# Kernel tuning notes

Measured on AMD Instinct MI355X. Metric: run time of the kernel, lower is better.

The kernel has to match this reference:

```python
import jax, jax.numpy as jnp
import numpy as np

B, T, D_MODEL, H = 2, 2048, 1024, 16
D_HEAD = D_MODEL // H


def setup_inputs() -> dict:
    key = jax.random.key(0)
    k1, k2, k3 = jax.random.split(key, 3)
    x = jax.random.normal(k1, (B, T, D_MODEL), dtype=jnp.float32)
    # Linear weights stored as (in, out); scale like torch default init roughly
    W_qkv = jax.random.normal(k2, (D_MODEL, 3 * D_MODEL), dtype=jnp.float32) / np.sqrt(D_MODEL)
    W_o = jax.random.normal(k3, (D_MODEL, D_MODEL), dtype=jnp.float32) / np.sqrt(D_MODEL)
    return {"x": x, "W_qkv": W_qkv, "W_o": W_o}


def reference(x, W_qkv, W_o):
    Bx, Tx, C = x.shape
    qkv = x @ W_qkv                                   # (B,T,3C)
    qkv = qkv.reshape(Bx, Tx, 3, H, D_HEAD)
    q = qkv[:, :, 0].transpose(0, 2, 1, 3)            # (B,H,T,D)
    k = qkv[:, :, 1].transpose(0, 2, 1, 3)
    v = qkv[:, :, 2].transpose(0, 2, 1, 3)
    scale = 1.0 / np.sqrt(D_HEAD).astype(np.float32)
    att = jnp.einsum('bhqd,bhkd->bhqk', q, k) * scale  # (B,H,T,T)
    causal = jnp.tril(jnp.ones((Tx, Tx), dtype=bool))
    att = jnp.where(causal[None, None], att, jnp.float32(-jnp.inf))
    w = jax.nn.softmax(att, axis=-1)
    out = jnp.einsum('bhqk,bhkd->bhqd', w, v)          # (B,H,T,D)
    out = out.transpose(0, 2, 1, 3).reshape(Bx, Tx, C)
    return out @ W_o
```

## Files before the change

kernel.cpp:

```cpp
#include <hip/hip_runtime.h>

typedef unsigned short u16;
typedef unsigned int u32;
typedef __bf16 bf16x8 __attribute__((ext_vector_type(8)));
typedef float f32x4 __attribute__((ext_vector_type(4)));

#define DEV __device__ __forceinline__

constexpr int BB = 2;
constexpr int TT = 2048;
constexpr int CD = 1024;
constexpr int HH = 16;
constexpr int DH = 64;
constexpr int BT = BB * TT;

#define QSCALE 0.18033688011112042f

DEV u16 f2bf(float f) {
    return __builtin_bit_cast(u16, (__bf16)f);
}

DEV f32x4 mfma16(bf16x8 a, bf16x8 b, f32x4 c) {
    return __builtin_amdgcn_mfma_f32_16x16x32_bf16(a, b, c, 0, 0, 0);
}

DEV void gld_lds16(u16* lds, const u16* g) {
    __builtin_amdgcn_global_load_lds(
        (const __attribute__((address_space(1))) unsigned int*)g,
        (__attribute__((address_space(3))) unsigned int*)lds, 16, 0, 0);
}

__global__ __launch_bounds__(256)
void prep_kernel(const float* __restrict__ x, u16* __restrict__ xb,
                 const float* __restrict__ Wqkv, u16* __restrict__ WqkvT,
                 const float* __restrict__ Wo, u16* __restrict__ WoT) {
    const int tid = threadIdx.x;
    int blk = blockIdx.x;
    if (blk < 2048) {
        const int i = (blk * 256 + tid) * 8;
        float4 a = *(const float4*)&x[i];
        float4 b = *(const float4*)&x[i + 4];
        u16 t[8];
        t[0] = f2bf(a.x); t[1] = f2bf(a.y); t[2] = f2bf(a.z); t[3] = f2bf(a.w);
        t[4] = f2bf(b.x); t[5] = f2bf(b.y); t[6] = f2bf(b.z); t[7] = f2bf(b.w);
        *(uint4*)&xb[i] = *(const uint4*)t;
        return;
    }
    __shared__ u16 tile[32][33];
    const float* in; u16* out; int rows, cols, bx, by;
    if (blk < 5120) { blk -= 2048; in = Wqkv; out = WqkvT; rows = 1024; cols = 3072; bx = blk % 96; by = blk / 96; }
    else            { blk -= 5120; in = Wo;   out = WoT;   rows = 1024; cols = 1024; bx = blk % 32; by = blk / 32; }
    const int c0 = bx * 32, r0 = by * 32;
    const int tx = tid & 31, ty = tid >> 5;
    #pragma unroll
    for (int i = ty; i < 32; i += 8)
        tile[i][tx] = f2bf(in[(r0 + i) * cols + (c0 + tx)]);
    __syncthreads();
    #pragma unroll
    for (int i = ty; i < 32; i += 8)
        out[(c0 + i) * rows + (r0 + tx)] = tile[tx][i];
}

template <int EPI, int BN, int GX>
__global__ __launch_bounds__(256)
void gemm_db(const u16* __restrict__ A, const u16* __restrict__ Bt,
             u16* __restrict__ out0, u16* __restrict__ out1,
             u16* __restrict__ out2, float* __restrict__ outf,
             int M, int N, int K) {
    constexpr int BM = 128, BK = 32, AST = 32;
    constexpr int NT = BN / 32;
    constexpr int NBLK = GX * 32;
    constexpr int CPX = NBLK / 8;
    __shared__ alignas(16) u16 As[3][BM * AST];
    __shared__ alignas(16) u16 Bs[3][BN * AST];

    const int tid  = threadIdx.x;
    const int wave = tid >> 6, lane = tid & 63;
    const int quad = lane >> 4, l16 = lane & 15;
    const int wm = (wave & 1) * 64, wn = (wave >> 1) * (BN / 2);

    int bid = (int)blockIdx.x;
    bid = (bid & 7) * CPX + (bid >> 3);
    const int bx = bid % GX, by = bid / GX;
    const int m0 = by * BM, n0 = bx * BN;

    const int srowA = wave * 32 + (lane >> 2);
    const int srowB = wave * (BN / 4) + (lane >> 2);
    const int scol  = (((lane & 3) ^ ((lane >> 3) & 3))) * 8;
    const u16* ga0 = A  + (size_t)(m0 + srowA) * K + scol;
    const u16* ga1 = ga0 + (size_t)16 * K;
    const u16* gb0 = Bt + (size_t)(n0 + srowB) * K + scol;
    const u16* gb1 = gb0 + (size_t)16 * K;

    auto stage = [&](int buf, int k0) {
        gld_lds16(&As[buf][wave * 1024],           ga0 + k0);
        gld_lds16(&As[buf][wave * 1024 + 512],     ga1 + k0);
        gld_lds16(&Bs[buf][wave * (BN * 8)],       gb0 + k0);
        if constexpr (BN == 128)
            gld_lds16(&Bs[buf][wave * (BN * 8) + 512], gb1 + k0);
    };
    auto wait_lps = [&]() {
        if constexpr (BN == 128) asm volatile("s_waitcnt vmcnt(4)" ::: "memory");
        else                     asm volatile("s_waitcnt vmcnt(3)" ::: "memory");
    };

    f32x4 acc[4][NT] = {};

    stage(0, 0);
    stage(1, BK);
    wait_lps();
    __builtin_amdgcn_s_barrier();

    const int sx = ((l16 >> 1) & 3) * 8;
    const int NS = K / BK;
    int cb = 0;
    for (int t = 0; t < NS; ++t) {
        const bool pf = (t + 2 < NS);
        int sb = cb + 2; if (sb >= 3) sb -= 3;
        if (pf) stage(sb, (t + 2) * BK);

        bf16x8 fa[4], fb[NT];
        #pragma unroll
        for (int mt = 0; mt < 4; ++mt)
            fa[mt] = *(const bf16x8*)
                &As[cb][(wm + mt * 16 + l16) * AST + (quad * 8 ^ sx)];
        #pragma unroll
        for (int nt = 0; nt < NT; ++nt)
            fb[nt] = *(const bf16x8*)
                &Bs[cb][(wn + nt * 16 + l16) * AST + (quad * 8 ^ sx)];
        #pragma unroll
        for (int mt = 0; mt < 4; ++mt)
            #pragma unroll
            for (int nt = 0; nt < NT; ++nt)
                acc[mt][nt] = mfma16(fa[mt], fb[nt], acc[mt][nt]);

        if (pf) wait_lps();
        else    asm volatile("s_waitcnt vmcnt(0)" ::: "memory");
        __builtin_amdgcn_s_barrier();
        cb = (cb + 1 == 3) ? 0 : cb + 1;
    }

    #pragma unroll
    for (int mt = 0; mt < 4; ++mt) {
        #pragma unroll
        for (int nt = 0; nt < NT; ++nt) {
            #pragma unroll
            for (int reg = 0; reg < 4; ++reg) {
                const int r = m0 + wm + mt * 16 + quad * 4 + reg;
                const int c = n0 + wn + nt * 16 + l16;
                if (EPI == 0) {
                    outf[(size_t)r * N + c] = acc[mt][nt][reg];
                } else {
                    const int which = c >> 10;
                    const int cc = c & 1023;
                    const int h = cc >> 6, d = cc & 63;
                    const int b = r >> 11, t = r & 2047;
                    const int bh = b * HH + h;
                    if (which == 0) {
                        out0[((size_t)bh * TT + t) * DH + d] =
                            f2bf(acc[mt][nt][reg] * QSCALE);
                    } else if (which == 1) {
                        out1[((size_t)bh * TT + t) * DH + d] = f2bf(acc[mt][nt][reg]);
                    } else {
                        out2[((size_t)bh * DH + d) * TT + t] = f2bf(acc[mt][nt][reg]);
                    }
                }
            }
        }
    }
}

constexpr int KST = 72;

DEV void attn_step(const bf16x8 fk[4][2], const bf16x8 fv[2][4],
                   const bf16x8* fq, f32x4* Oacc,
                   float& m_i, float& l_i, bool diag,
                   int wave, int quad, int l16) {
    f32x4 st[4];
    #pragma unroll
    for (int nt = 0; nt < 4; ++nt) {
        f32x4 t = {};
        t = mfma16(fk[nt][0], fq[0], t);
        t = mfma16(fk[nt][1], fq[1], t);
        st[nt] = t;
    }

    if (diag) {
        const int qg = wave * 16 + l16;
        #pragma unroll
        for (int nt = 0; nt < 4; ++nt)
            #pragma unroll
            for (int reg = 0; reg < 4; ++reg) {
                const int kg = nt * 16 + quad * 4 + reg;
                st[nt][reg] = (kg <= qg) ? st[nt][reg] : -INFINITY;
            }
    }

    float v[16];
    #pragma unroll
    for (int nt = 0; nt < 4; ++nt)
        #pragma unroll
        for (int reg = 0; reg < 4; ++reg)
            v[nt * 4 + reg] = st[nt][reg];
    #pragma unroll
    for (int s = 8; s > 0; s >>= 1)
        #pragma unroll
        for (int i = 0; i < s; ++i)
            v[i] = fmaxf(v[i], v[i + s]);
    float vmax = v[0];
    vmax = fmaxf(vmax, __shfl_xor(vmax, 16, 64));
    vmax = fmaxf(vmax, __shfl_xor(vmax, 32, 64));

    const float mnew = fmaxf(m_i, vmax);
    const float alpha = __builtin_amdgcn_exp2f(m_i - mnew);
    m_i = mnew;

    #pragma unroll
    for (int nt = 0; nt < 4; ++nt)
        #pragma unroll
        for (int reg = 0; reg < 4; ++reg) {
            const float p = __builtin_amdgcn_exp2f(st[nt][reg] - mnew);
            st[nt][reg] = p;
            v[nt * 4 + reg] = p;
        }
    #pragma unroll
    for (int s = 8; s > 0; s >>= 1)
        #pragma unroll
        for (int i = 0; i < s; ++i)
            v[i] += v[i + s];
    float vsum = v[0];
    vsum += __shfl_xor(vsum, 16, 64);
    vsum += __shfl_xor(vsum, 32, 64);
    l_i = l_i * alpha + vsum;

    #pragma unroll
    for (int dt = 0; dt < 4; ++dt)
        #pragma unroll
        for (int reg = 0; reg < 4; ++reg)
            Oacc[dt][reg] *= alpha;

    #pragma unroll
    for (int pair = 0; pair < 2; ++pair) {
        bf16x8 pb;
        #pragma unroll
        for (int j = 0; j < 4; ++j) {
            pb[j]     = (__bf16)st[2 * pair][j];
            pb[4 + j] = (__bf16)st[2 * pair + 1][j];
        }
        #pragma unroll
        for (int dt = 0; dt < 4; ++dt)
            Oacc[dt] = mfma16(fv[pair][dt], pb, Oacc[dt]);
    }
}

__global__ __launch_bounds__(256, 4)
void attn_kernel(const u16* __restrict__ Q, const u16* __restrict__ Kb,
                 const u16* __restrict__ Vt, u16* __restrict__ O) {
    __shared__ alignas(16) u16 Ks[2][64 * KST];
    __shared__ alignas(16) u16 Vs[2][64 * KST];

    const int bid = (int)blockIdx.x;
    const int j2 = bid >> 3;
    const int qt = 31 - (j2 >> 2);
    const int bh = (bid & 7) + 8 * (j2 & 3);
    const int jmax = qt;

    const int tid = threadIdx.x;
    const int wave = tid >> 6, lane = tid & 63;
    const int quad = lane >> 4, l16 = lane & 15;

    const u16* Qh = Q  + (size_t)bh * TT * DH;
    const u16* Kh = Kb + (size_t)bh * TT * DH;
    const u16* Vh = Vt + (size_t)bh * DH * TT;

    const int row = qt * 64 + wave * 16;

    bf16x8 fq[2];
    fq[0] = *(const bf16x8*)&Qh[(row + l16) * DH + quad * 8];
    fq[1] = *(const bf16x8*)&Qh[(row + l16) * DH + 32 + quad * 8];

    f32x4 Oa[4] = {};
    float m_i = -INFINITY, l_i = 0.f;

    const int trow = tid >> 3;
    const int ic   = tid & 7;
    const int tcol = ic * 8;
    const int vc1 = 32 * (ic >> 2) + 16 * (ic & 1) + 4 * ((ic & 3) >> 1);
    uint4 kr0, kr1, vr0, vr1;

    auto load_chunk = [&](int j) {
        const u16* ks = Kh + (size_t)j * 64 * DH;
        kr0 = *(const uint4*)&ks[trow * DH + tcol];
        kr1 = *(const uint4*)&ks[(trow + 32) * DH + tcol];
        const u16* vs = Vh + (size_t)j * 64;
        vr0 = *(const uint4*)&vs[(size_t)trow * TT + tcol];
        vr1 = *(const uint4*)&vs[(size_t)(trow + 32) * TT + tcol];
    };
    auto write_chunk = [&](int buf) {
        *(uint4*)&Ks[buf][trow * KST + tcol]        = kr0;
        *(uint4*)&Ks[buf][(trow + 32) * KST + tcol] = kr1;
        *(uint2*)&Vs[buf][trow * KST + vc1]            = *(const uint2*)&vr0;
        *(uint2*)&Vs[buf][trow * KST + vc1 + 8]        = *((const uint2*)&vr0 + 1);
        *(uint2*)&Vs[buf][(trow + 32) * KST + vc1]     = *(const uint2*)&vr1;
        *(uint2*)&Vs[buf][(trow + 32) * KST + vc1 + 8] = *((const uint2*)&vr1 + 1);
    };

    load_chunk(0);
    write_chunk(0);

    for (int j = 0; j <= jmax; ++j) {
        const int cur = j & 1;
        __syncthreads();
        if (j < jmax) load_chunk(j + 1);

        bf16x8 fk[4][2], fv[2][4];
        #pragma unroll
        for (int nt = 0; nt < 4; ++nt) {
            fk[nt][0] = *(const bf16x8*)&Ks[cur][(nt * 16 + l16) * KST + quad * 8];
            fk[nt][1] = *(const bf16x8*)&Ks[cur][(nt * 16 + l16) * KST + 32 + quad * 8];
        }
        #pragma unroll
        for (int pair = 0; pair < 2; ++pair)
            #pragma unroll
            for (int dt = 0; dt < 4; ++dt)
                fv[pair][dt] = *(const bf16x8*)
                    &Vs[cur][(dt * 16 + l16) * KST + pair * 32 + quad * 8];

        attn_step(fk, fv, fq, Oa, m_i, l_i, (j == qt), wave, quad, l16);
        if (j < jmax) write_chunk(cur ^ 1);
    }

    const int b = bh >> 4, h = bh & 15;
    const float r_i = 1.f / l_i;
    #pragma unroll
    for (int dt = 0; dt < 4; ++dt) {
        u16 oa[4];
        #pragma unroll
        for (int reg = 0; reg < 4; ++reg)
            oa[reg] = f2bf(Oa[dt][reg] * r_i);
        *(uint2*)&O[((size_t)(b * TT + row + l16)) * CD + h * DH + dt * 16 + quad * 4] =
            *(const uint2*)oa;
    }
}

extern "C" void kernel_launch(void* const* d_in, const int* in_sizes, int n_in,
                              void* d_out, int out_size, void* d_ws, size_t ws_size,
                              hipStream_t stream) {
    (void)in_sizes; (void)n_in; (void)out_size; (void)ws_size;
    const float* x    = (const float*)d_in[0];
    const float* Wqkv = (const float*)d_in[1];
    const float* Wo   = (const float*)d_in[2];
    float* out = (float*)d_out;

    char* ws = (char*)d_ws;
    u16* xb    = (u16*)(ws + 0);
    u16* WqkvT = (u16*)(ws + (8u  << 20));
    u16* WoT   = (u16*)(ws + (14u << 20));
    u16* Qb    = (u16*)(ws + (16u << 20));
    u16* Kb    = (u16*)(ws + (24u << 20));
    u16* Vt    = (u16*)(ws + (32u << 20));
    u16* attn  = (u16*)(ws + (40u << 20));

    prep_kernel<<<6144, 256, 0, stream>>>(x, xb, Wqkv, WqkvT, Wo, WoT);

    gemm_db<1, 128, 24><<<768, 256, 0, stream>>>(
        xb, WqkvT, Qb, Kb, Vt, nullptr, BT, 3072, CD);

    attn_kernel<<<1024, 256, 0, stream>>>(Qb, Kb, Vt, attn);

    gemm_db<0, 64, 16><<<512, 256, 0, stream>>>(
        attn, WoT, nullptr, nullptr, nullptr, out, BT, CD, CD);
}
```

Before: 179.5 us.

## Process two query tiles per attention block to share K/V shared-memory loads

Each attention block now handles two adjacent 64-row query tiles (128 rows) against the same staged K/V chunks. Each K and V fragment read from shared memory therefore feeds MFMAs for both tiles, which halves K/V global and LDS traffic per query row. The grid shrinks from 1024 to 512 blocks, with a new scheduling order that pairs heavy and light causal tiles. Launch bounds drop to 2 waves per SIMD to make room for the doubled register state, which lowers occupancy and latency hiding.

```diff
diff --git a/kernel.cpp b/kernel.cpp
--- a/kernel.cpp
+++ b/kernel.cpp
@@ -172,21 +172,9 @@
 
 constexpr int KST = 72;
 
-DEV void attn_step(const bf16x8 fk[4][2], const bf16x8 fv[2][4],
-                   const bf16x8* fq, f32x4* Oacc,
-                   float& m_i, float& l_i, bool diag,
-                   int wave, int quad, int l16) {
-    f32x4 st[4];
-    #pragma unroll
-    for (int nt = 0; nt < 4; ++nt) {
-        f32x4 t = {};
-        t = mfma16(fk[nt][0], fq[0], t);
-        t = mfma16(fk[nt][1], fq[1], t);
-        st[nt] = t;
-    }
-
+DEV void softmax_half(f32x4* st, f32x4* Oacc, float& m_i, float& l_i,
+                      bool diag, int quad, int qg) {
     if (diag) {
-        const int qg = wave * 16 + l16;
         #pragma unroll
         for (int nt = 0; nt < 4; ++nt)
             #pragma unroll
@@ -195,7 +183,6 @@
                 st[nt][reg] = (kg <= qg) ? st[nt][reg] : -INFINITY;
             }
     }
-
     float v[16];
     #pragma unroll
     for (int nt = 0; nt < 4; ++nt)
@@ -238,32 +225,19 @@
         #pragma unroll
         for (int reg = 0; reg < 4; ++reg)
             Oacc[dt][reg] *= alpha;
-
-    #pragma unroll
-    for (int pair = 0; pair < 2; ++pair) {
-        bf16x8 pb;
-        #pragma unroll
-        for (int j = 0; j < 4; ++j) {
-            pb[j]     = (__bf16)st[2 * pair][j];
-            pb[4 + j] = (__bf16)st[2 * pair + 1][j];
-        }
-        #pragma unroll
-        for (int dt = 0; dt < 4; ++dt)
-            Oacc[dt] = mfma16(fv[pair][dt], pb, Oacc[dt]);
-    }
-}
-
-__global__ __launch_bounds__(256, 4)
+}
+
+__global__ __launch_bounds__(256, 2)
 void attn_kernel(const u16* __restrict__ Q, const u16* __restrict__ Kb,
                  const u16* __restrict__ Vt, u16* __restrict__ O) {
     __shared__ alignas(16) u16 Ks[2][64 * KST];
     __shared__ alignas(16) u16 Vs[2][64 * KST];
 
     const int bid = (int)blockIdx.x;
-    const int j2 = bid >> 3;
-    const int qt = 31 - (j2 >> 2);
-    const int bh = (bid & 7) + 8 * (j2 & 3);
-    const int jmax = qt;
+    const int bh = bid & 31;
+    const int q  = (bid < 256) ? 15 - (bid >> 5) : (bid >> 5) - 8;
+    const int jA = 2 * q;
+    const int jB = 2 * q + 1;
 
     const int tid = threadIdx.x;
     const int wave = tid >> 6, lane = tid & 63;
@@ -273,14 +247,17 @@
     const u16* Kh = Kb + (size_t)bh * TT * DH;
     const u16* Vh = Vt + (size_t)bh * DH * TT;
 
-    const int row = qt * 64 + wave * 16;
-
-    bf16x8 fq[2];
-    fq[0] = *(const bf16x8*)&Qh[(row + l16) * DH + quad * 8];
-    fq[1] = *(const bf16x8*)&Qh[(row + l16) * DH + 32 + quad * 8];
-
-    f32x4 Oa[4] = {};
-    float m_i = -INFINITY, l_i = 0.f;
+    const int rowA = q * 128 + wave * 16;
+    const int rowB = q * 128 + 64 + wave * 16;
+
+    bf16x8 fqA[2], fqB[2];
+    fqA[0] = *(const bf16x8*)&Qh[(rowA + l16) * DH + quad * 8];
+    fqA[1] = *(const bf16x8*)&Qh[(rowA + l16) * DH + 32 + quad * 8];
+    fqB[0] = *(const bf16x8*)&Qh[(rowB + l16) * DH + quad * 8];
+    fqB[1] = *(const bf16x8*)&Qh[(rowB + l16) * DH + 32 + quad * 8];
+
+    f32x4 OaA[4] = {}, OaB[4] = {};
+    float mA = -INFINITY, lA = 0.f, mB = -INFINITY, lB = 0.f;
 
     const int trow = tid >> 3;
     const int ic   = tid & 7;
@@ -308,38 +285,71 @@
     load_chunk(0);
     write_chunk(0);
 
-    for (int j = 0; j <= jmax; ++j) {
+    for (int j = 0; j <= jB; ++j) {
         const int cur = j & 1;
         __syncthreads();
-        if (j < jmax) load_chunk(j + 1);
-
-        bf16x8 fk[4][2], fv[2][4];
+        if (j < jB) load_chunk(j + 1);
+
+        const bool doA = (j <= jA);
+        const u16* Kc = Ks[cur];
+        const u16* Vc = Vs[cur];
+
+        f32x4 sA[4], sB[4];
         #pragma unroll
         for (int nt = 0; nt < 4; ++nt) {
-            fk[nt][0] = *(const bf16x8*)&Ks[cur][(nt * 16 + l16) * KST + quad * 8];
-            fk[nt][1] = *(const bf16x8*)&Ks[cur][(nt * 16 + l16) * KST + 32 + quad * 8];
-        }
-        #pragma unroll
-        for (int pair = 0; pair < 2; ++pair)
-            #pragma unroll
-            for (int dt = 0; dt < 4; ++dt)
-                fv[pair][dt] = *(const bf16x8*)
-                    &Vs[cur][(dt * 16 + l16) * KST + pair * 32 + quad * 8];
-
-        attn_step(fk, fv, fq, Oa, m_i, l_i, (j == qt), wave, quad, l16);
-        if (j < jmax) write_chunk(cur ^ 1);
+            const bf16x8 k0 = *(const bf16x8*)&Kc[(nt * 16 + l16) * KST + quad * 8];
+            const bf16x8 k1 = *(const bf16x8*)&Kc[(nt * 16 + l16) * KST + 32 + quad * 8];
+            if (doA) {
+                f32x4 t = {};
+                t = mfma16(k0, fqA[0], t);
+                t = mfma16(k1, fqA[1], t);
+                sA[nt] = t;
+            }
+            f32x4 u = {};
+            u = mfma16(k0, fqB[0], u);
+            u = mfma16(k1, fqB[1], u);
+            sB[nt] = u;
+        }
+
+        if (doA) softmax_half(sA, OaA, mA, lA, (j == jA), quad, wave * 16 + l16);
+        softmax_half(sB, OaB, mB, lB, (j == jB), quad, wave * 16 + l16);
+
+        #pragma unroll
+        for (int pair = 0; pair < 2; ++pair) {
+            bf16x8 pbA, pbB;
+            #pragma unroll
+            for (int jj = 0; jj < 4; ++jj) {
+                pbA[jj]     = (__bf16)sA[2 * pair][jj];
+                pbA[4 + jj] = (__bf16)sA[2 * pair + 1][jj];
+                pbB[jj]     = (__bf16)sB[2 * pair][jj];
+                pbB[4 + jj] = (__bf16)sB[2 * pair + 1][jj];
+            }
+            #pragma unroll
+            for (int dt = 0; dt < 4; ++dt) {
+                const bf16x8 fvd = *(const bf16x8*)
+                    &Vc[(dt * 16 + l16) * KST + pair * 32 + quad * 8];
+                if (doA) OaA[dt] = mfma16(fvd, pbA, OaA[dt]);
+                OaB[dt] = mfma16(fvd, pbB, OaB[dt]);
+            }
+        }
+
+        if (j < jB) write_chunk(cur ^ 1);
     }
 
     const int b = bh >> 4, h = bh & 15;
-    const float r_i = 1.f / l_i;
+    const float rA = 1.f / lA, rB = 1.f / lB;
     #pragma unroll
     for (int dt = 0; dt < 4; ++dt) {
-        u16 oa[4];
-        #pragma unroll
-        for (int reg = 0; reg < 4; ++reg)
-            oa[reg] = f2bf(Oa[dt][reg] * r_i);
-        *(uint2*)&O[((size_t)(b * TT + row + l16)) * CD + h * DH + dt * 16 + quad * 4] =
+        u16 oa[4], ob[4];
+        #pragma unroll
+        for (int reg = 0; reg < 4; ++reg) {
+            oa[reg] = f2bf(OaA[dt][reg] * rA);
+            ob[reg] = f2bf(OaB[dt][reg] * rB);
+        }
+        *(uint2*)&O[((size_t)(b * TT + rowA + l16)) * CD + h * DH + dt * 16 + quad * 4] =
             *(const uint2*)oa;
+        *(uint2*)&O[((size_t)(b * TT + rowB + l16)) * CD + h * DH + dt * 16 + quad * 4] =
+            *(const uint2*)ob;
     }
 }
 
@@ -366,7 +376,7 @@
     gemm_db<1, 128, 24><<<768, 256, 0, stream>>>(
         xb, WqkvT, Qb, Kb, Vt, nullptr, BT, 3072, CD);
 
-    attn_kernel<<<1024, 256, 0, stream>>>(Qb, Kb, Vt, attn);
+    attn_kernel<<<512, 256, 0, stream>>>(Qb, Kb, Vt, attn);
 
     gemm_db<0, 64, 16><<<512, 256, 0, stream>>>(
         attn, WoT, nullptr, nullptr, nullptr, out, BT, CD, CD);
```

Measured after the change: 181.0 us. About the same (+0.8%).

## Split long causal query tiles across two blocks and merge with a combine kernel

Applied to the files above, without the earlier changes.

Query tiles 16-31 have their key range split in two halves handled by separate blocks that write fp32 partial outputs and running max/sum to workspace. A new combine kernel rescales and merges each pair into the bf16 attention output. A task table orders the work so long and short tiles are paired to balance load across the 1536 blocks. This trades an extra launch and fp32 partial-output traffic for less tail imbalance from the longest causal rows. The split path is used only when the workspace is large enough, otherwise the original kernel runs.

```diff
diff --git a/kernel.cpp b/kernel.cpp
--- a/kernel.cpp
+++ b/kernel.cpp
@@ -172,6 +172,15 @@
 
 constexpr int KST = 72;
 
+__device__ const unsigned char TQT[48] = {
+    31,31,30,15,  30,29,29,28,14,  28,27,27,26,13,  26,25,25,24,12,
+    24,23,23,22,11,  22,21,21,20,10,  20,19,19,18,9,  18,17,17,16,8,
+    16,7,  6,5,4,3,2,1,0};
+__device__ const unsigned char TMODE[48] = {
+    0,1,0,2,  1,0,1,0,2,  1,0,1,0,2,  1,0,1,0,2,
+    1,0,1,0,2,  1,0,1,0,2,  1,0,1,0,2,  1,0,1,0,2,
+    1,2,  2,2,2,2,2,2,2};
+
 DEV void attn_step(const bf16x8 fk[4][2], const bf16x8 fv[2][4],
                    const bf16x8* fq, f32x4* Oacc,
                    float& m_i, float& l_i, bool diag,
@@ -253,17 +262,29 @@
     }
 }
 
+template <int SPLIT>
 __global__ __launch_bounds__(256, 4)
 void attn_kernel(const u16* __restrict__ Q, const u16* __restrict__ Kb,
-                 const u16* __restrict__ Vt, u16* __restrict__ O) {
+                 const u16* __restrict__ Vt, u16* __restrict__ O,
+                 float* __restrict__ Opart, float* __restrict__ MLpart) {
     __shared__ alignas(16) u16 Ks[2][64 * KST];
     __shared__ alignas(16) u16 Vs[2][64 * KST];
 
     const int bid = (int)blockIdx.x;
-    const int j2 = bid >> 3;
-    const int qt = 31 - (j2 >> 2);
-    const int bh = (bid & 7) + 8 * (j2 & 3);
-    const int jmax = qt;
+    int qt, mode, bh;
+    if (SPLIT) {
+        const int task = bid >> 5;
+        qt = TQT[task]; mode = TMODE[task];
+        bh = bid & 31;
+    } else {
+        qt = 31 - (bid >> 5); mode = 2;
+        bh = (bid & 7) + 8 * ((bid >> 3) & 3);
+    }
+    const int c0 = (qt + 2) >> 1;
+    int j0 = 0, j1 = qt;
+    bool hasdiag = true;
+    if (SPLIT && mode == 0) { j1 = c0 - 1; hasdiag = false; }
+    if (SPLIT && mode == 1) { j0 = c0; }
 
     const int tid = threadIdx.x;
     const int wave = tid >> 6, lane = tid & 63;
@@ -305,13 +326,13 @@
         *(uint2*)&Vs[buf][(trow + 32) * KST + vc1 + 8] = *((const uint2*)&vr1 + 1);
     };
 
-    load_chunk(0);
+    load_chunk(j0);
     write_chunk(0);
 
-    for (int j = 0; j <= jmax; ++j) {
-        const int cur = j & 1;
+    for (int j = j0; j <= j1; ++j) {
+        const int cur = (j - j0) & 1;
         __syncthreads();
-        if (j < jmax) load_chunk(j + 1);
+        if (j < j1) load_chunk(j + 1);
 
         bf16x8 fk[4][2], fv[2][4];
         #pragma unroll
@@ -326,27 +347,77 @@
                 fv[pair][dt] = *(const bf16x8*)
                     &Vs[cur][(dt * 16 + l16) * KST + pair * 32 + quad * 8];
 
-        attn_step(fk, fv, fq, Oa, m_i, l_i, (j == qt), wave, quad, l16);
-        if (j < jmax) write_chunk(cur ^ 1);
-    }
-
+        attn_step(fk, fv, fq, Oa, m_i, l_i, hasdiag && (j == qt),
+                  wave, quad, l16);
+        if (j < j1) write_chunk(cur ^ 1);
+    }
+
+    if (!SPLIT || mode == 2) {
+        const int b = bh >> 4, h = bh & 15;
+        const float r_i = 1.f / l_i;
+        #pragma unroll
+        for (int dt = 0; dt < 4; ++dt) {
+            u16 oa[4];
+            #pragma unroll
+            for (int reg = 0; reg < 4; ++reg)
+                oa[reg] = f2bf(Oa[dt][reg] * r_i);
+            *(uint2*)&O[((size_t)(b * TT + row + l16)) * CD + h * DH + dt * 16 + quad * 4] =
+                *(const uint2*)oa;
+        }
+    } else {
+        const int pidx = ((qt - 16) * 32 + bh) * 2 + mode;
+        float* Op = Opart + (size_t)pidx * 4096;
+        #pragma unroll
+        for (int dt = 0; dt < 4; ++dt)
+            #pragma unroll
+            for (int reg = 0; reg < 4; ++reg)
+                Op[(dt * 16 + quad * 4 + reg) * 64 + wave * 16 + l16] = Oa[dt][reg];
+        if (quad == 0) {
+            MLpart[pidx * 128 + wave * 16 + l16]      = m_i;
+            MLpart[pidx * 128 + 64 + wave * 16 + l16] = l_i;
+        }
+    }
+}
+
+__global__ __launch_bounds__(256)
+void attn_combine(const float* __restrict__ Opart,
+                  const float* __restrict__ MLpart, u16* __restrict__ O) {
+    const int pair = (int)blockIdx.x;
+    const int qti = pair >> 5, bh = pair & 31;
+    const int qt = 16 + qti;
+    const int pbase = (qti * 32 + bh) * 2;
+    const float* O0 = Opart + (size_t)pbase * 4096;
+    const float* O1 = O0 + 4096;
+    const float* ml0 = MLpart + pbase * 128;
+    const float* ml1 = ml0 + 128;
+
+    const int tid = threadIdx.x;
+    const int rrow = tid >> 2;
+    const int d0 = (tid & 3) * 16;
+
+    const float m0 = ml0[rrow], l0 = ml0[64 + rrow];
+    const float m1 = ml1[rrow], l1 = ml1[64 + rrow];
+    const float M = fmaxf(m0, m1);
+    const float w0 = __builtin_amdgcn_exp2f(m0 - M);
+    const float w1 = __builtin_amdgcn_exp2f(m1 - M);
+    const float rL = 1.f / (l0 * w0 + l1 * w1);
+
+    u16 o[16];
+    #pragma unroll
+    for (int i = 0; i < 16; ++i) {
+        const int d = d0 + i;
+        o[i] = f2bf((O0[d * 64 + rrow] * w0 + O1[d * 64 + rrow] * w1) * rL);
+    }
     const int b = bh >> 4, h = bh & 15;
-    const float r_i = 1.f / l_i;
-    #pragma unroll
-    for (int dt = 0; dt < 4; ++dt) {
-        u16 oa[4];
-        #pragma unroll
-        for (int reg = 0; reg < 4; ++reg)
-            oa[reg] = f2bf(Oa[dt][reg] * r_i);
-        *(uint2*)&O[((size_t)(b * TT + row + l16)) * CD + h * DH + dt * 16 + quad * 4] =
-            *(const uint2*)oa;
-    }
+    u16* dst = &O[((size_t)(b * TT + qt * 64 + rrow)) * CD + h * DH + d0];
+    *(uint4*)dst = *(const uint4*)o;
+    *(uint4*)(dst + 8) = *((const uint4*)o + 1);
 }
 
 extern "C" void kernel_launch(void* const* d_in, const int* in_sizes, int n_in,
                               void* d_out, int out_size, void* d_ws, size_t ws_size,
                               hipStream_t stream) {
-    (void)in_sizes; (void)n_in; (void)out_size; (void)ws_size;
+    (void)in_sizes; (void)n_in; (void)out_size;
     const float* x    = (const float*)d_in[0];
     const float* Wqkv = (const float*)d_in[1];
     const float* Wo   = (const float*)d_in[2];
@@ -360,13 +431,20 @@
     u16* Kb    = (u16*)(ws + (24u << 20));
     u16* Vt    = (u16*)(ws + (32u << 20));
     u16* attn  = (u16*)(ws + (40u << 20));
+    float* Opart  = (float*)(ws + (48u << 20));
+    float* MLpart = (float*)(ws + (65u << 20));
 
     prep_kernel<<<6144, 256, 0, stream>>>(x, xb, Wqkv, WqkvT, Wo, WoT);
 
     gemm_db<1, 128, 24><<<768, 256, 0, stream>>>(
         xb, WqkvT, Qb, Kb, Vt, nullptr, BT, 3072, CD);
 
-    attn_kernel<<<1024, 256, 0, stream>>>(Qb, Kb, Vt, attn);
+    if (ws_size >= (66u << 20)) {
+        attn_kernel<1><<<1536, 256, 0, stream>>>(Qb, Kb, Vt, attn, Opart, MLpart);
+        attn_combine<<<512, 256, 0, stream>>>(Opart, MLpart, attn);
+    } else {
+        attn_kernel<0><<<1024, 256, 0, stream>>>(Qb, Kb, Vt, attn, nullptr, nullptr);
+    }
 
     gemm_db<0, 64, 16><<<512, 256, 0, stream>>>(
         attn, WoT, nullptr, nullptr, nullptr, out, BT, CD, CD);
```

Result: no change. 181.5 us (+1.1%).

## Skip softmax rescale lazily and compute row sums via MFMA with ones

Applied to the files above, without the earlier changes.

Replaces the per-step online-softmax rescale with a lazy rescale that only runs when some row's max grows by more than a threshold, checked wave-wide. The row-sum reduction (tree add plus cross-lane shuffles) is replaced by an extra MFMA that multiplies the bf16 probabilities by a ones vector into a separate accumulator. This removes shuffles and VALU work from the inner loop, in exchange for one extra MFMA per pair and for summing rounded bf16 probabilities. The lazy max threshold relies on exp2 values staying bounded by 2^8.

```diff
diff --git a/kernel.cpp b/kernel.cpp
--- a/kernel.cpp
+++ b/kernel.cpp
@@ -173,8 +173,8 @@
 constexpr int KST = 72;
 
 DEV void attn_step(const bf16x8 fk[4][2], const bf16x8 fv[2][4],
-                   const bf16x8* fq, f32x4* Oacc,
-                   float& m_i, float& l_i, bool diag,
+                   const bf16x8 fone, const bf16x8* fq,
+                   f32x4* Oacc, f32x4& lacc, float& m_i, bool diag,
                    int wave, int quad, int l16) {
     f32x4 st[4];
     #pragma unroll
@@ -211,33 +211,25 @@
     vmax = fmaxf(vmax, __shfl_xor(vmax, 16, 64));
     vmax = fmaxf(vmax, __shfl_xor(vmax, 32, 64));
 
-    const float mnew = fmaxf(m_i, vmax);
-    const float alpha = __builtin_amdgcn_exp2f(m_i - mnew);
-    m_i = mnew;
+    if (!__all(vmax - m_i <= 8.f)) {
+        const float mnew = fmaxf(m_i, vmax);
+        const float alpha = __builtin_amdgcn_exp2f(m_i - mnew);
+        m_i = mnew;
+        #pragma unroll
+        for (int dt = 0; dt < 4; ++dt)
+            #pragma unroll
+            for (int reg = 0; reg < 4; ++reg)
+                Oacc[dt][reg] *= alpha;
+        #pragma unroll
+        for (int reg = 0; reg < 4; ++reg)
+            lacc[reg] *= alpha;
+    }
 
     #pragma unroll
     for (int nt = 0; nt < 4; ++nt)
         #pragma unroll
-        for (int reg = 0; reg < 4; ++reg) {
-            const float p = __builtin_amdgcn_exp2f(st[nt][reg] - mnew);
-            st[nt][reg] = p;
-            v[nt * 4 + reg] = p;
-        }
-    #pragma unroll
-    for (int s = 8; s > 0; s >>= 1)
-        #pragma unroll
-        for (int i = 0; i < s; ++i)
-            v[i] += v[i + s];
-    float vsum = v[0];
-    vsum += __shfl_xor(vsum, 16, 64);
-    vsum += __shfl_xor(vsum, 32, 64);
-    l_i = l_i * alpha + vsum;
-
-    #pragma unroll
-    for (int dt = 0; dt < 4; ++dt)
-        #pragma unroll
         for (int reg = 0; reg < 4; ++reg)
-            Oacc[dt][reg] *= alpha;
+            st[nt][reg] = __builtin_amdgcn_exp2f(st[nt][reg] - m_i);
 
     #pragma unroll
     for (int pair = 0; pair < 2; ++pair) {
@@ -247,6 +239,7 @@
             pb[j]     = (__bf16)st[2 * pair][j];
             pb[4 + j] = (__bf16)st[2 * pair + 1][j];
         }
+        lacc = mfma16(fone, pb, lacc);
         #pragma unroll
         for (int dt = 0; dt < 4; ++dt)
             Oacc[dt] = mfma16(fv[pair][dt], pb, Oacc[dt]);
@@ -279,8 +272,15 @@
     fq[0] = *(const bf16x8*)&Qh[(row + l16) * DH + quad * 8];
     fq[1] = *(const bf16x8*)&Qh[(row + l16) * DH + 32 + quad * 8];
 
-    f32x4 Oa[4] = {};
-    float m_i = -INFINITY, l_i = 0.f;
+    bf16x8 fone;
+    {
+        const __bf16 ov = (l16 == 0) ? (__bf16)1.f : (__bf16)0.f;
+        #pragma unroll
+        for (int j = 0; j < 8; ++j) fone[j] = ov;
+    }
+
+    f32x4 Oa[4] = {}, lacc = {};
+    float m_i = -INFINITY;
 
     const int trow = tid >> 3;
     const int ic   = tid & 7;
@@ -326,12 +326,15 @@
                 fv[pair][dt] = *(const bf16x8*)
                     &Vs[cur][(dt * 16 + l16) * KST + pair * 32 + quad * 8];
 
-        attn_step(fk, fv, fq, Oa, m_i, l_i, (j == qt), wave, quad, l16);
+        attn_step(fk, fv, fone, fq, Oa, lacc, m_i, (j == qt),
+                  wave, quad, l16);
         if (j < jmax) write_chunk(cur ^ 1);
     }
 
+    const float lrow = __shfl(lacc[0], l16, 64);
+    const float r_i = 1.f / lrow;
+
     const int b = bh >> 4, h = bh & 15;
-    const float r_i = 1.f / l_i;
     #pragma unroll
     for (int dt = 0; dt < 4; ++dt) {
         u16 oa[4];
```

New measurement: 175.5 us. -2.2%, faster.
